# Optimization experiments

Hardware: AMD Instinct MI355X
Metric: run time of the kernel (lower is better)

Reference implementation:

```python
import jax, jax.numpy as jnp
import numpy as np

N_USER, N_FOOD, N_ING, N_CAT, N_HAB = 50000, 30000, 20000, 5000, 10000
N_NODES = N_USER + N_FOOD + N_ING + N_CAT + N_HAB  # 115000
N_REL = 8
COMMON = 128
HIDDEN = 128
N_CLASSES = 2
N_EDGES = 1500000


def setup_inputs() -> dict:
    key = jax.random.key(0)
    ks = jax.random.split(key, 24)

    def lin(k, din, dout):
        k1, k2 = jax.random.split(k)
        s = 1.0 / np.sqrt(din)
        W = jax.random.uniform(k1, (din, dout), jnp.float32, -s, s)
        b = jax.random.uniform(k2, (dout,), jnp.float32, -s, s)
        return W, b

    Wu, bu = lin(ks[0], 256, COMMON)
    Wf, bf = lin(ks[1], 512, COMMON)
    Wi, bi = lin(ks[2], 128, COMMON)
    Wc, bc = lin(ks[3], 64, COMMON)
    Wh, bh = lin(ks[4], 64, COMMON)

    s1 = 1.0 / np.sqrt(COMMON)
    W1 = jax.random.uniform(ks[5], (N_REL, COMMON, HIDDEN), jnp.float32, -s1, s1)
    root1 = jax.random.uniform(ks[6], (COMMON, HIDDEN), jnp.float32, -s1, s1)
    b1 = jnp.zeros((HIDDEN,), jnp.float32)

    s2 = 1.0 / np.sqrt(HIDDEN)
    W2 = jax.random.uniform(ks[7], (N_REL, HIDDEN, N_CLASSES), jnp.float32, -s2, s2)
    root2 = jax.random.uniform(ks[8], (HIDDEN, N_CLASSES), jnp.float32, -s2, s2)
    b2 = jnp.zeros((N_CLASSES,), jnp.float32)

    return {
        "x_user": jax.random.normal(ks[9], (N_USER, 256), jnp.float32),
        "x_food": jax.random.normal(ks[10], (N_FOOD, 512), jnp.float32),
        "x_ingredient": jax.random.normal(ks[11], (N_ING, 128), jnp.float32),
        "x_category": jax.random.normal(ks[12], (N_CAT, 64), jnp.float32),
        "x_habit": jax.random.normal(ks[13], (N_HAB, 64), jnp.float32),
        "Wu": Wu, "bu": bu, "Wf": Wf, "bf": bf, "Wi": Wi, "bi": bi,
        "Wc": Wc, "bc": bc, "Wh": Wh, "bh": bh,
        "W1": W1, "root1": root1, "b1": b1,
        "W2": W2, "root2": root2, "b2": b2,
        "edge_index": jax.random.randint(ks[14], (2, N_EDGES), 0, N_NODES, jnp.int64),
        "edge_type": jax.random.randint(ks[15], (N_EDGES,), 0, N_REL, jnp.int64),
    }


def rgcn_conv(x, src, dst, etype, W, root, bias):
    # x: [N, Din]; W: [R, Din, Dout]. Per-relation node transform, then
    # per-edge gather + per-(dst, relation) mean aggregation (PyG RGCNConv, aggr='mean').
    N = x.shape[0]
    R = W.shape[0]
    h = jnp.einsum('nd,rdf->nrf', x, W)            # [N, R, Dout]
    msgs = h[src, etype]                           # [E, Dout]
    seg = dst * R + etype                          # combined (dst, relation) segment id
    sums = jax.ops.segment_sum(msgs, seg, num_segments=N * R)
    cnt = jax.ops.segment_sum(jnp.ones((src.shape[0],), x.dtype), seg, num_segments=N * R)
    mean = sums / jnp.maximum(cnt, 1.0)[:, None]   # [N*R, Dout]
    agg = mean.reshape(N, R, -1).sum(axis=1)       # sum over relations
    return agg + x @ root + bias


def reference(x_user, x_food, x_ingredient, x_category, x_habit,
              Wu, bu, Wf, bf, Wi, bi, Wc, bc, Wh, bh,
              W1, root1, b1, W2, root2, b2,
              edge_index, edge_type):
    x_all = jnp.concatenate([
        x_user @ Wu + bu,
        x_food @ Wf + bf,
        x_ingredient @ Wi + bi,
        x_category @ Wc + bc,
        x_habit @ Wh + bh,
    ], axis=0)                                     # [N, COMMON]
    src, dst = edge_index[0], edge_index[1]
    x = rgcn_conv(x_all, src, dst, edge_type, W1, root1, b1)
    x = jax.nn.relu(x)                             # dropout is identity in eval mode
    x = rgcn_conv(x, src, dst, edge_type, W2, root2, b2)
    return jax.nn.log_softmax(x, axis=1)
```

## Files before the change

### kernel.cpp

```cpp
#include <hip/hip_runtime.h>
#include <hip/hip_bf16.h>
#include <math.h>

#define NU 50000
#define NFOOD 30000
#define NING 20000
#define NCAT 5000
#define NHAB 10000
#define NNODES 115000
#define NCHUNK 14375
#define NREL 8
#define NSEG (NNODES * NREL)
#define NEDGE 1500000
#define SCAN_B 256

typedef __attribute__((ext_vector_type(8))) short short8;
typedef __attribute__((ext_vector_type(4))) float f32x4;

static inline size_t alignup(size_t x) { return (x + 255) & ~(size_t)255; }

__device__ inline float bf16_bits_to_f32(unsigned short u) {
  return __uint_as_float(((unsigned)u) << 16);
}
__device__ inline unsigned short f32_to_bf16_bits(float f) {
  unsigned u = __float_as_uint(f);
  unsigned r = u + 0x7fffu + ((u >> 16) & 1u);
  return (unsigned short)(r >> 16);
}
__device__ inline unsigned pack_bf16x2(float lo, float hi) {
  return (unsigned)f32_to_bf16_bits(lo) | ((unsigned)f32_to_bf16_bits(hi) << 16);
}

template <bool A_F32, bool OUT_BF16, bool RELU_OUT>
__global__ __launch_bounds__(256) void mfma_gemm(
    const void* __restrict__ Ain, const unsigned short* __restrict__ Bt, int ldB,
    const float* __restrict__ bias, void* __restrict__ Cv, int ldC, int Nstore,
    int M, int N, int K) {
  __shared__ char As[128 * 128];
  __shared__ char Bs[128 * 128];
  const int tid = threadIdx.x;
  const int lane = tid & 63;
  const int wv = tid >> 6;
  const int bm = blockIdx.y * 128;
  const int bn = blockIdx.x * 128;
  f32x4 acc[2][8] = {};

  for (int k0 = 0; k0 < K; k0 += 64) {
    if (A_F32) {
      const float* A = (const float*)Ain;
#pragma unroll
      for (int it = 0; it < 4; ++it) {
        int u = it * 256 + tid;
        int m = u >> 3, c = u & 7;
        int mg = bm + m; if (mg >= M) mg = M - 1;
        const float4* src = (const float4*)(A + (size_t)mg * K + k0 + c * 8);
        float4 lo4 = src[0], hi4 = src[1];
        unsigned q0 = pack_bf16x2(lo4.x, lo4.y);
        unsigned q1 = pack_bf16x2(lo4.z, lo4.w);
        unsigned q2 = pack_bf16x2(hi4.x, hi4.y);
        unsigned q3 = pack_bf16x2(hi4.z, hi4.w);
        int off = m * 128 + ((c * 16) ^ ((m & 7) << 4));
        *(int4*)(As + off) = make_int4(q0, q1, q2, q3);
      }
    } else {
      const unsigned short* A = (const unsigned short*)Ain;
#pragma unroll
      for (int it = 0; it < 4; ++it) {
        int u = it * 256 + tid;
        int m = u >> 3, c = u & 7;
        int mg = bm + m; if (mg >= M) mg = M - 1;
        int4 v = *(const int4*)((const char*)(A + (size_t)mg * K + k0) + c * 16);
        int off = m * 128 + ((c * 16) ^ ((m & 7) << 4));
        *(int4*)(As + off) = v;
      }
    }
#pragma unroll
    for (int it = 0; it < 4; ++it) {
      int u = it * 256 + tid;
      int n = u >> 3, c = u & 7;
      int4 v = *(const int4*)((const char*)(Bt + (size_t)(bn + n) * ldB + k0) + c * 16);
      int off = n * 128 + ((c * 16) ^ ((n & 7) << 4));
      *(int4*)(Bs + off) = v;
    }
    __syncthreads();
#pragma unroll
    for (int kk = 0; kk < 2; ++kk) {
      int kbyte = kk * 64 + ((lane >> 4) << 4);
      short8 af[2];
#pragma unroll
      for (int mi = 0; mi < 2; ++mi) {
        int m = wv * 32 + mi * 16 + (lane & 15);
        af[mi] = *(const short8*)(As + m * 128 + (kbyte ^ ((m & 7) << 4)));
      }
#pragma unroll
      for (int ni = 0; ni < 8; ++ni) {
        int n = ni * 16 + (lane & 15);
        short8 bf = *(const short8*)(Bs + n * 128 + (kbyte ^ ((n & 7) << 4)));
#pragma unroll
        for (int mi = 0; mi < 2; ++mi)
          acc[mi][ni] = __builtin_amdgcn_mfma_f32_16x16x32_bf16(af[mi], bf, acc[mi][ni], 0, 0, 0);
      }
    }
    __syncthreads();
  }
#pragma unroll
  for (int mi = 0; mi < 2; ++mi) {
#pragma unroll
    for (int r = 0; r < 4; ++r) {
      int row = bm + wv * 32 + mi * 16 + ((lane >> 4) << 2) + r;
      if (row < M) {
#pragma unroll
        for (int ni = 0; ni < 8; ++ni) {
          int col = bn + ni * 16 + (lane & 15);
          if (col < Nstore) {
            float v = acc[mi][ni][r] + (bias ? bias[col] : 0.f);
            if (RELU_OUT) v = fmaxf(v, 0.f);
            if (OUT_BF16)
              ((unsigned short*)Cv)[(size_t)row * ldC + col] = f32_to_bf16_bits(v);
            else
              ((float*)Cv)[(size_t)row * ldC + col] = v;
          }
        }
      }
    }
  }
}

struct ProjP {
  const float *A0, *A1, *A2, *A3, *A4;
  const float *b0, *b1, *b2, *b3, *b4;
  int t1, t2, t3, t4;
};

__global__ __launch_bounds__(256) void proj_all(ProjP P, const unsigned short* __restrict__ Wp,
                                                unsigned short* __restrict__ x_all) {
  __shared__ char As[128 * 128];
  __shared__ char Bs[128 * 128];
  const int by = blockIdx.y;
  const int tid = threadIdx.x;
  const int lane = tid & 63;
  const int wv = tid >> 6;
  const float* A; const float* bias;
  int M, K, Woff, tile0; long Coff;
  if (by < P.t1)      { A = P.A0; bias = P.b0; M = NU;    K = 256; Woff = 0;      Coff = 0;                 tile0 = 0; }
  else if (by < P.t2) { A = P.A1; bias = P.b1; M = NFOOD; K = 512; Woff = 32768;  Coff = (long)NU * 128;    tile0 = P.t1; }
  else if (by < P.t3) { A = P.A2; bias = P.b2; M = NING;  K = 128; Woff = 98304;  Coff = (long)(NU+NFOOD)*128; tile0 = P.t2; }
  else if (by < P.t4) { A = P.A3; bias = P.b3; M = NCAT;  K = 64;  Woff = 114688; Coff = (long)(NU+NFOOD+NING)*128; tile0 = P.t3; }
  else                { A = P.A4; bias = P.b4; M = NHAB;  K = 64;  Woff = 122880; Coff = (long)(NU+NFOOD+NING+NCAT)*128; tile0 = P.t4; }
  const unsigned short* Bt = Wp + Woff;
  const int bm = (by - tile0) * 128;
  f32x4 acc[2][8] = {};

  for (int k0 = 0; k0 < K; k0 += 64) {
#pragma unroll
    for (int it = 0; it < 4; ++it) {
      int u = it * 256 + tid;
      int m = u >> 3, c = u & 7;
      int mg = bm + m; if (mg >= M) mg = M - 1;
      const float4* src = (const float4*)(A + (size_t)mg * K + k0 + c * 8);
      float4 lo4 = src[0], hi4 = src[1];
      unsigned q0 = pack_bf16x2(lo4.x, lo4.y);
      unsigned q1 = pack_bf16x2(lo4.z, lo4.w);
      unsigned q2 = pack_bf16x2(hi4.x, hi4.y);
      unsigned q3 = pack_bf16x2(hi4.z, hi4.w);
      int off = m * 128 + ((c * 16) ^ ((m & 7) << 4));
      *(int4*)(As + off) = make_int4(q0, q1, q2, q3);
    }
#pragma unroll
    for (int it = 0; it < 4; ++it) {
      int u = it * 256 + tid;
      int n = u >> 3, c = u & 7;
      int4 v = *(const int4*)((const char*)(Bt + (size_t)n * K + k0) + c * 16);
      int off = n * 128 + ((c * 16) ^ ((n & 7) << 4));
      *(int4*)(Bs + off) = v;
    }
    __syncthreads();
#pragma unroll
    for (int kk = 0; kk < 2; ++kk) {
      int kbyte = kk * 64 + ((lane >> 4) << 4);
      short8 af[2];
#pragma unroll
      for (int mi = 0; mi < 2; ++mi) {
        int m = wv * 32 + mi * 16 + (lane & 15);
        af[mi] = *(const short8*)(As + m * 128 + (kbyte ^ ((m & 7) << 4)));
      }
#pragma unroll
      for (int ni = 0; ni < 8; ++ni) {
        int n = ni * 16 + (lane & 15);
        short8 bf = *(const short8*)(Bs + n * 128 + (kbyte ^ ((n & 7) << 4)));
#pragma unroll
        for (int mi = 0; mi < 2; ++mi)
          acc[mi][ni] = __builtin_amdgcn_mfma_f32_16x16x32_bf16(af[mi], bf, acc[mi][ni], 0, 0, 0);
      }
    }
    __syncthreads();
  }
#pragma unroll
  for (int mi = 0; mi < 2; ++mi) {
#pragma unroll
    for (int r = 0; r < 4; ++r) {
      int row = bm + wv * 32 + mi * 16 + ((lane >> 4) << 2) + r;
      if (row < M) {
#pragma unroll
        for (int ni = 0; ni < 8; ++ni) {
          int col = ni * 16 + (lane & 15);
          float v = acc[mi][ni][r] + bias[col];
          x_all[Coff + (size_t)row * 128 + col] = f32_to_bf16_bits(v);
        }
      }
    }
  }
}

__global__ __launch_bounds__(256) void l1_gemm(
    const unsigned short* __restrict__ M9, const unsigned short* __restrict__ xall,
    const unsigned short* __restrict__ W1rT, const float* __restrict__ b1,
    unsigned short* __restrict__ x1, int d0, int Mc) {
  __shared__ char As[128 * 128];
  __shared__ char Bs[128 * 128];
  const int tid = threadIdx.x;
  const int lane = tid & 63;
  const int wv = tid >> 6;
  const int bm = blockIdx.y * 128;
  f32x4 acc[2][8] = {};

  for (int k0 = 0; k0 < 1152; k0 += 64) {
#pragma unroll
    for (int it = 0; it < 4; ++it) {
      int u = it * 256 + tid;
      int m = u >> 3, c = u & 7;
      int mg = bm + m; if (mg >= Mc) mg = Mc - 1;
      const char* src;
      if (k0 < 1024) src = (const char*)(M9 + (size_t)mg * 1024 + k0) + c * 16;
      else src = (const char*)(xall + (size_t)(d0 + mg) * 128 + (k0 - 1024)) + c * 16;
      int4 v = *(const int4*)src;
      int off = m * 128 + ((c * 16) ^ ((m & 7) << 4));
      *(int4*)(As + off) = v;
    }
#pragma unroll
    for (int it = 0; it < 4; ++it) {
      int u = it * 256 + tid;
      int n = u >> 3, c = u & 7;
      int4 v = *(const int4*)((const char*)(W1rT + (size_t)n * 1152 + k0) + c * 16);
      int off = n * 128 + ((c * 16) ^ ((n & 7) << 4));
      *(int4*)(Bs + off) = v;
    }
    __syncthreads();
#pragma unroll
    for (int kk = 0; kk < 2; ++kk) {
      int kbyte = kk * 64 + ((lane >> 4) << 4);
      short8 af[2];
#pragma unroll
      for (int mi = 0; mi < 2; ++mi) {
        int m = wv * 32 + mi * 16 + (lane & 15);
        af[mi] = *(const short8*)(As + m * 128 + (kbyte ^ ((m & 7) << 4)));
      }
#pragma unroll
      for (int ni = 0; ni < 8; ++ni) {
        int n = ni * 16 + (lane & 15);
        short8 bf = *(const short8*)(Bs + n * 128 + (kbyte ^ ((n & 7) << 4)));
#pragma unroll
        for (int mi = 0; mi < 2; ++mi)
          acc[mi][ni] = __builtin_amdgcn_mfma_f32_16x16x32_bf16(af[mi], bf, acc[mi][ni], 0, 0, 0);
      }
    }
    __syncthreads();
  }
#pragma unroll
  for (int mi = 0; mi < 2; ++mi) {
#pragma unroll
    for (int r = 0; r < 4; ++r) {
      int row = bm + wv * 32 + mi * 16 + ((lane >> 4) << 2) + r;
      if (row < Mc) {
#pragma unroll
        for (int ni = 0; ni < 8; ++ni) {
          int col = ni * 16 + (lane & 15);
          float v = fmaxf(acc[mi][ni][r] + b1[col], 0.f);
          x1[(size_t)(d0 + row) * 128 + col] = f32_to_bf16_bits(v);
        }
      }
    }
  }
}

__global__ void build_all(const float* __restrict__ Wu, const float* __restrict__ Wf,
                          const float* __restrict__ Wi, const float* __restrict__ Wc,
                          const float* __restrict__ Wh, const float* __restrict__ W1,
                          const float* __restrict__ root1, const float* __restrict__ W2,
                          const float* __restrict__ root2,
                          unsigned short* __restrict__ Wp,
                          unsigned short* __restrict__ W1rT,
                          unsigned short* __restrict__ B2pad,
                          int* __restrict__ cnt_dt) {
  const int T0 = 32768, T1 = T0 + 65536, T2 = T1 + 16384, T3 = T2 + 8192, T4 = T3 + 8192,
            T5 = T4 + 147456, T6 = T5 + 16384, T7 = T6 + NSEG;
  int i = blockIdx.x * blockDim.x + threadIdx.x;
  int stride = gridDim.x * blockDim.x;
  for (; i < T7; i += stride) {
    if (i < T0) {
      int n = i / 256, k = i - n * 256;
      Wp[i] = f32_to_bf16_bits(Wu[(size_t)k * 128 + n]);
    } else if (i < T1) {
      int j = i - T0; int n = j / 512, k = j - n * 512;
      Wp[i] = f32_to_bf16_bits(Wf[(size_t)k * 128 + n]);
    } else if (i < T2) {
      int j = i - T1; int n = j >> 7, k = j & 127;
      Wp[i] = f32_to_bf16_bits(Wi[(size_t)k * 128 + n]);
    } else if (i < T3) {
      int j = i - T2; int n = j >> 6, k = j & 63;
      Wp[i] = f32_to_bf16_bits(Wc[(size_t)k * 128 + n]);
    } else if (i < T4) {
      int j = i - T3; int n = j >> 6, k = j & 63;
      Wp[i] = f32_to_bf16_bits(Wh[(size_t)k * 128 + n]);
    } else if (i < T5) {
      int j = i - T4; int f = j / 1152, c = j - f * 1152;
      float v;
      if (c < 1024) { int t = c >> 7, k = c & 127; v = W1[((size_t)t * 128 + k) * 128 + f]; }
      else { int k = c - 1024; v = root1[(size_t)k * 128 + f]; }
      W1rT[j] = f32_to_bf16_bits(v);
    } else if (i < T6) {
      int j = i - T5; int n = j >> 7, k = j & 127;
      float v = 0.f;
      if (n < 16) v = W2[((size_t)(n >> 1) * 128 + k) * 2 + (n & 1)];
      else if (n < 18) v = root2[(size_t)k * 2 + (n - 16)];
      B2pad[j] = f32_to_bf16_bits(v);
    } else {
      cnt_dt[i - T6] = 0;
    }
  }
}

__global__ void count_dt_xcd(const int* __restrict__ ei, const int* __restrict__ et,
                             int* __restrict__ cnt_dt) {
  int cls = blockIdx.x & 7;
  unsigned lo = cls * NCHUNK, hi = lo + NCHUNK;
  int e = (blockIdx.x >> 3) * blockDim.x + threadIdx.x;
  int stride = (gridDim.x >> 3) * blockDim.x;
  for (; e < NEDGE; e += stride) {
    unsigned d = (unsigned)ei[NEDGE + e]; if (d >= NNODES) d = 0;
    if (d < lo || d >= hi) continue;
    unsigned t = (unsigned)et[e]; if (t >= NREL) t = 0;
    atomicAdd(cnt_dt + d * NREL + t, 1);
  }
}

__global__ void scan_block(const int* __restrict__ in, int* __restrict__ out,
                           int* __restrict__ bsum, int n) {
  __shared__ int s[SCAN_B];
  int i = blockIdx.x * SCAN_B + threadIdx.x;
  int x = (i < n) ? in[i] : 0;
  s[threadIdx.x] = x;
  __syncthreads();
  for (int d = 1; d < SCAN_B; d <<= 1) {
    int v = (threadIdx.x >= d) ? s[threadIdx.x - d] : 0;
    __syncthreads();
    s[threadIdx.x] += v;
    __syncthreads();
  }
  if (i < n) out[i] = s[threadIdx.x] - x;
  if (threadIdx.x == SCAN_B - 1) bsum[blockIdx.x] = s[threadIdx.x];
}

__global__ void scan_mid(const int* __restrict__ bsumA, int* __restrict__ bsumAs, int nb) {
  __shared__ int s[256];
  __shared__ int carry;
  if (threadIdx.x == 0) carry = 0;
  __syncthreads();
  for (int c0 = 0; c0 < nb; c0 += 256) {
    int i = c0 + threadIdx.x;
    int x = (i < nb) ? bsumA[i] : 0;
    s[threadIdx.x] = x;
    __syncthreads();
    for (int d = 1; d < 256; d <<= 1) {
      int v = (threadIdx.x >= d) ? s[threadIdx.x - d] : 0;
      __syncthreads();
      s[threadIdx.x] += v;
      __syncthreads();
    }
    if (i < nb) bsumAs[i] = carry + s[threadIdx.x] - x;
    __syncthreads();
    if (threadIdx.x == 255) carry += s[255];
    __syncthreads();
  }
}

__global__ void scan_apply2(int* __restrict__ rp2, const int* __restrict__ lvl1,
                            int* __restrict__ slot, int n) {
  int i = blockIdx.x * blockDim.x + threadIdx.x;
  if (i >= n) return;
  int v = rp2[i] + lvl1[i >> 8];
  rp2[i] = v;
  slot[i] = v;
}

__global__ void scatter_edges_xcd(const int* __restrict__ ei, const int* __restrict__ et,
                                  int* __restrict__ slot, unsigned* __restrict__ packed) {
  int cls = blockIdx.x & 7;
  unsigned lo = cls * NCHUNK, hi = lo + NCHUNK;
  int e = (blockIdx.x >> 3) * blockDim.x + threadIdx.x;
  int stride = (gridDim.x >> 3) * blockDim.x;
  for (; e < NEDGE; e += stride) {
    unsigned d = (unsigned)ei[NEDGE + e]; if (d >= NNODES) d = 0;
    if (d < lo || d >= hi) continue;
    unsigned s = (unsigned)ei[e];  if (s >= NNODES) s = 0;
    unsigned t = (unsigned)et[e];  if (t >= NREL)  t = 0;
    int pos = atomicAdd(slot + d * NREL + t, 1);
    packed[pos] = s;
  }
}

__global__ __launch_bounds__(256) void gather_rounds(
    const int* __restrict__ rp2, const unsigned* __restrict__ packed,
    const int4* __restrict__ xu, unsigned* __restrict__ M9, int d0, int d1) {
  const int lane = threadIdx.x & 63;
  const int qtr = lane >> 4;
  const int sub = lane & 15;
  int wid = (blockIdx.x * blockDim.x + threadIdx.x) >> 6;
  int nw = (gridDim.x * blockDim.x) >> 6;
  for (int p0 = d0 + wid * 4; p0 < d1; p0 += nw * 4) {
    int d = p0 + qtr;
    bool valid = (d < d1);
    int bi = (valid ? d : d0) * NREL;
    int b[9];
#pragma unroll
    for (int q = 0; q < 9; ++q)
      b[q] = (bi + q == NSEG) ? NEDGE : rp2[bi + q];
    int len[8];
    int mx = 0;
#pragma unroll
    for (int q = 0; q < 8; ++q) {
      len[q] = valid ? (b[q + 1] - b[q]) : 0;
      mx = len[q] > mx ? len[q] : mx;
    }
    float a[8][8];
#pragma unroll
    for (int q = 0; q < 8; ++q)
#pragma unroll
      for (int j = 0; j < 8; ++j) a[q][j] = 0.f;
    for (int r = 0; r < mx; ++r) {
#pragma unroll
      for (int q = 0; q < 8; ++q) {
        if (r < len[q]) {
          int4 v = xu[(size_t)packed[b[q] + r] * 16 + sub];
          unsigned u0 = (unsigned)v.x, u1 = (unsigned)v.y;
          unsigned u2 = (unsigned)v.z, u3 = (unsigned)v.w;
          a[q][0] += bf16_bits_to_f32((unsigned short)(u0 & 0xffffu));
          a[q][1] += bf16_bits_to_f32((unsigned short)(u0 >> 16));
          a[q][2] += bf16_bits_to_f32((unsigned short)(u1 & 0xffffu));
          a[q][3] += bf16_bits_to_f32((unsigned short)(u1 >> 16));
          a[q][4] += bf16_bits_to_f32((unsigned short)(u2 & 0xffffu));
          a[q][5] += bf16_bits_to_f32((unsigned short)(u2 >> 16));
          a[q][6] += bf16_bits_to_f32((unsigned short)(u3 & 0xffffu));
          a[q][7] += bf16_bits_to_f32((unsigned short)(u3 >> 16));
        }
      }
    }
    if (valid) {
      unsigned* rowp = M9 + (size_t)(d - d0) * 512;
#pragma unroll
      for (int q = 0; q < 8; ++q) {
        float w = 1.0f / (float)(len[q] > 0 ? len[q] : 1);
        uint4 o;
        o.x = pack_bf16x2(a[q][0] * w, a[q][1] * w);
        o.y = pack_bf16x2(a[q][2] * w, a[q][3] * w);
        o.z = pack_bf16x2(a[q][4] * w, a[q][5] * w);
        o.w = pack_bf16x2(a[q][6] * w, a[q][7] * w);
        *(uint4*)(rowp + q * 64 + sub * 4) = o;
      }
    }
  }
}

__global__ void fused_out(const int* __restrict__ rp2, const unsigned* __restrict__ packed,
                          const float* __restrict__ h2, const float* __restrict__ b2,
                          float* __restrict__ out) {
  int gt = blockIdx.x * blockDim.x + threadIdx.x;
  int d = gt >> 2;
  int l4 = gt & 3;
  if (d >= NNODES) return;
  float z0 = 0.f, z1 = 0.f;
#pragma unroll
  for (int k = 0; k < 2; ++k) {
    int t = l4 * 2 + k;
    int i = d * NREL + t;
    int beg = rp2[i];
    int end = (i == NSEG - 1) ? NEDGE : rp2[i + 1];
    float s0 = 0.f, s1 = 0.f;
    for (int e = beg; e < end; ++e) {
      unsigned s = packed[e];
      s0 += h2[(size_t)s * 18 + t * 2];
      s1 += h2[(size_t)s * 18 + t * 2 + 1];
    }
    int c = end - beg;
    float w = 1.0f / (float)(c > 0 ? c : 1);
    z0 += s0 * w;
    z1 += s1 * w;
  }
  z0 += __shfl_xor(z0, 1, 4); z0 += __shfl_xor(z0, 2, 4);
  z1 += __shfl_xor(z1, 1, 4); z1 += __shfl_xor(z1, 2, 4);
  if (l4 == 0) {
    z0 += h2[(size_t)d * 18 + 16] + b2[0];
    z1 += h2[(size_t)d * 18 + 17] + b2[1];
    float m = fmaxf(z0, z1);
    float l = m + logf(expf(z0 - m) + expf(z1 - m));
    out[(size_t)d * 2 + 0] = z0 - l;
    out[(size_t)d * 2 + 1] = z1 - l;
  }
}

__global__ void fill_sentinel(float* __restrict__ out, int n, float v) {
  int i = blockIdx.x * blockDim.x + threadIdx.x;
  if (i < n) out[i] = v;
}

extern "C" void kernel_launch(void* const* d_in, const int* in_sizes, int n_in,
                              void* d_out, int out_size, void* d_ws, size_t ws_size,
                              hipStream_t stream) {
  const float* x_user = (const float*)d_in[0];
  const float* x_food = (const float*)d_in[1];
  const float* x_ing  = (const float*)d_in[2];
  const float* x_cat  = (const float*)d_in[3];
  const float* x_hab  = (const float*)d_in[4];
  const float* Wu = (const float*)d_in[5];  const float* bu  = (const float*)d_in[6];
  const float* Wf = (const float*)d_in[7];  const float* bfo = (const float*)d_in[8];
  const float* Wi = (const float*)d_in[9];  const float* bi  = (const float*)d_in[10];
  const float* Wc = (const float*)d_in[11]; const float* bc  = (const float*)d_in[12];
  const float* Wh = (const float*)d_in[13]; const float* bh  = (const float*)d_in[14];
  const float* W1 = (const float*)d_in[15]; const float* root1 = (const float*)d_in[16];
  const float* b1 = (const float*)d_in[17];
  const float* W2 = (const float*)d_in[18]; const float* root2 = (const float*)d_in[19];
  const float* b2 = (const float*)d_in[20];
  const int* ei = (const int*)d_in[21];
  const int* et = (const int*)d_in[22];
  (void)in_sizes; (void)n_in;

  dim3 blk(256);
  const int NB_A = (NSEG + SCAN_B - 1) / SCAN_B;

  char* ws = (char*)d_ws;
  size_t off = 0;
  unsigned short* x_all = (unsigned short*)(ws + off); off += alignup((size_t)NNODES * 128 * 2);
  unsigned short* x1    = (unsigned short*)(ws + off); off += alignup((size_t)NNODES * 128 * 2);
  int* cnt_dt = (int*)(ws + off);        off += alignup((size_t)NSEG * 4);
  int* rp2 = (int*)(ws + off);           off += alignup((size_t)NSEG * 4);
  int* slot = (int*)(ws + off);          off += alignup((size_t)NSEG * 4);
  unsigned* packed = (unsigned*)(ws + off); off += alignup((size_t)NEDGE * 4);
  int* bsumA = (int*)(ws + off);         off += alignup((size_t)4096 * 4);
  int* bsumAs = (int*)(ws + off);        off += alignup((size_t)4096 * 4);
  unsigned short* Wp = (unsigned short*)(ws + off);   off += alignup((size_t)131072 * 2);
  unsigned short* W1rT = (unsigned short*)(ws + off); off += alignup((size_t)128 * 1152 * 2);
  unsigned short* B2pad = (unsigned short*)(ws + off); off += alignup((size_t)128 * 128 * 2);
  float* h2 = (float*)(ws + off);        off += alignup((size_t)NNODES * 18 * 4);
  size_t base = off;

  int NCH = 0;
  for (int cand = 1; cand <= 16; cand <<= 1) {
    size_t ch = ((size_t)NNODES + cand - 1) / cand;
    if (base + alignup(ch * 1024 * 2) <= ws_size) { NCH = cand; break; }
  }
  if (NCH == 0) {
    fill_sentinel<<<(out_size + 255) / 256, blk, 0, stream>>>((float*)d_out, out_size, -777.0f);
    return;
  }
  unsigned short* M9 = (unsigned short*)(ws + base);
  const int CH = (NNODES + NCH - 1) / NCH;

  build_all<<<2048, blk, 0, stream>>>(Wu, Wf, Wi, Wc, Wh, W1, root1, W2, root2,
                                      Wp, W1rT, B2pad, cnt_dt);

  {
    ProjP P;
    P.A0 = x_user; P.A1 = x_food; P.A2 = x_ing; P.A3 = x_cat; P.A4 = x_hab;
    P.b0 = bu; P.b1 = bfo; P.b2 = bi; P.b3 = bc; P.b4 = bh;
    P.t1 = 391; P.t2 = 391 + 235; P.t3 = 391 + 235 + 157; P.t4 = 391 + 235 + 157 + 40;
    int ntiles = P.t4 + 79;
    proj_all<<<dim3(1, ntiles), blk, 0, stream>>>(P, Wp, x_all);
  }

  count_dt_xcd<<<2048, blk, 0, stream>>>(ei, et, cnt_dt);
  scan_block<<<NB_A, SCAN_B, 0, stream>>>(cnt_dt, rp2, bsumA, NSEG);
  scan_mid<<<1, 256, 0, stream>>>(bsumA, bsumAs, NB_A);
  scan_apply2<<<NB_A, SCAN_B, 0, stream>>>(rp2, bsumAs, slot, NSEG);
  scatter_edges_xcd<<<2048, blk, 0, stream>>>(ei, et, slot, packed);

  for (int c = 0; c < NCH; ++c) {
    int d0 = c * CH;
    int d1 = (d0 + CH < NNODES) ? d0 + CH : NNODES;
    int Mc = d1 - d0;
    int groups = (Mc + 3) / 4;
    int gblocks = (groups + 3) / 4;
    gather_rounds<<<gblocks, blk, 0, stream>>>(rp2, packed, (const int4*)x_all,
                                               (unsigned*)M9, d0, d1);
    dim3 g(1, (Mc + 127) / 128);
    l1_gemm<<<g, blk, 0, stream>>>(M9, x_all, W1rT, b1, x1, d0, Mc);
  }

  { dim3 g(1, (NNODES + 127) / 128);
    mfma_gemm<false, false, false><<<g, blk, 0, stream>>>(x1, B2pad, 128, nullptr, (void*)h2, 18, 18, NNODES, 128, 128); }

  fused_out<<<(NNODES * 4 + 255) / 256, blk, 0, stream>>>(rp2, packed, h2, b2, (float*)d_out);
}
```

Before: 479.4 us.

## Fuse layer-2 projection GEMM into layer-1 GEMM epilogue via shared memory

The layer-1 GEMM now keeps its ReLU'd bf16 output tile in shared memory, reusing the A/B staging buffers. It multiplies that tile by the padded layer-2 weights loaded into LDS and writes h2 directly. This removes the x1 intermediate (write plus reread of about 29 MB) and one kernel launch. In exchange it adds LDS usage and extra per-block work after the main loop, which may reduce occupancy.

```diff
diff --git a/kernel.cpp b/kernel.cpp
--- a/kernel.cpp
+++ b/kernel.cpp
@@ -29,101 +29,6 @@
 }
 __device__ inline unsigned pack_bf16x2(float lo, float hi) {
   return (unsigned)f32_to_bf16_bits(lo) | ((unsigned)f32_to_bf16_bits(hi) << 16);
-}
-
-template <bool A_F32, bool OUT_BF16, bool RELU_OUT>
-__global__ __launch_bounds__(256) void mfma_gemm(
-    const void* __restrict__ Ain, const unsigned short* __restrict__ Bt, int ldB,
-    const float* __restrict__ bias, void* __restrict__ Cv, int ldC, int Nstore,
-    int M, int N, int K) {
-  __shared__ char As[128 * 128];
-  __shared__ char Bs[128 * 128];
-  const int tid = threadIdx.x;
-  const int lane = tid & 63;
-  const int wv = tid >> 6;
-  const int bm = blockIdx.y * 128;
-  const int bn = blockIdx.x * 128;
-  f32x4 acc[2][8] = {};
-
-  for (int k0 = 0; k0 < K; k0 += 64) {
-    if (A_F32) {
-      const float* A = (const float*)Ain;
-#pragma unroll
-      for (int it = 0; it < 4; ++it) {
-        int u = it * 256 + tid;
-        int m = u >> 3, c = u & 7;
-        int mg = bm + m; if (mg >= M) mg = M - 1;
-        const float4* src = (const float4*)(A + (size_t)mg * K + k0 + c * 8);
-        float4 lo4 = src[0], hi4 = src[1];
-        unsigned q0 = pack_bf16x2(lo4.x, lo4.y);
-        unsigned q1 = pack_bf16x2(lo4.z, lo4.w);
-        unsigned q2 = pack_bf16x2(hi4.x, hi4.y);
-        unsigned q3 = pack_bf16x2(hi4.z, hi4.w);
-        int off = m * 128 + ((c * 16) ^ ((m & 7) << 4));
-        *(int4*)(As + off) = make_int4(q0, q1, q2, q3);
-      }
-    } else {
-      const unsigned short* A = (const unsigned short*)Ain;
-#pragma unroll
-      for (int it = 0; it < 4; ++it) {
-        int u = it * 256 + tid;
-        int m = u >> 3, c = u & 7;
-        int mg = bm + m; if (mg >= M) mg = M - 1;
-        int4 v = *(const int4*)((const char*)(A + (size_t)mg * K + k0) + c * 16);
-        int off = m * 128 + ((c * 16) ^ ((m & 7) << 4));
-        *(int4*)(As + off) = v;
-      }
-    }
-#pragma unroll
-    for (int it = 0; it < 4; ++it) {
-      int u = it * 256 + tid;
-      int n = u >> 3, c = u & 7;
-      int4 v = *(const int4*)((const char*)(Bt + (size_t)(bn + n) * ldB + k0) + c * 16);
-      int off = n * 128 + ((c * 16) ^ ((n & 7) << 4));
-      *(int4*)(Bs + off) = v;
-    }
-    __syncthreads();
-#pragma unroll
-    for (int kk = 0; kk < 2; ++kk) {
-      int kbyte = kk * 64 + ((lane >> 4) << 4);
-      short8 af[2];
-#pragma unroll
-      for (int mi = 0; mi < 2; ++mi) {
-        int m = wv * 32 + mi * 16 + (lane & 15);
-        af[mi] = *(const short8*)(As + m * 128 + (kbyte ^ ((m & 7) << 4)));
-      }
-#pragma unroll
-      for (int ni = 0; ni < 8; ++ni) {
-        int n = ni * 16 + (lane & 15);
-        short8 bf = *(const short8*)(Bs + n * 128 + (kbyte ^ ((n & 7) << 4)));
-#pragma unroll
-        for (int mi = 0; mi < 2; ++mi)
-          acc[mi][ni] = __builtin_amdgcn_mfma_f32_16x16x32_bf16(af[mi], bf, acc[mi][ni], 0, 0, 0);
-      }
-    }
-    __syncthreads();
-  }
-#pragma unroll
-  for (int mi = 0; mi < 2; ++mi) {
-#pragma unroll
-    for (int r = 0; r < 4; ++r) {
-      int row = bm + wv * 32 + mi * 16 + ((lane >> 4) << 2) + r;
-      if (row < M) {
-#pragma unroll
-        for (int ni = 0; ni < 8; ++ni) {
-          int col = bn + ni * 16 + (lane & 15);
-          if (col < Nstore) {
-            float v = acc[mi][ni][r] + (bias ? bias[col] : 0.f);
-            if (RELU_OUT) v = fmaxf(v, 0.f);
-            if (OUT_BF16)
-              ((unsigned short*)Cv)[(size_t)row * ldC + col] = f32_to_bf16_bits(v);
-            else
-              ((float*)Cv)[(size_t)row * ldC + col] = v;
-          }
-        }
-      }
-    }
-  }
 }
 
 struct ProjP {
@@ -215,14 +120,24 @@
 __global__ __launch_bounds__(256) void l1_gemm(
     const unsigned short* __restrict__ M9, const unsigned short* __restrict__ xall,
     const unsigned short* __restrict__ W1rT, const float* __restrict__ b1,
-    unsigned short* __restrict__ x1, int d0, int Mc) {
+    const unsigned short* __restrict__ B2pad, float* __restrict__ h2,
+    int d0, int Mc) {
   __shared__ char As[128 * 128];
   __shared__ char Bs[128 * 128];
+  __shared__ char B2s[32 * 256];
   const int tid = threadIdx.x;
   const int lane = tid & 63;
   const int wv = tid >> 6;
+  const int r16 = lane & 15;
+  const int q0 = lane >> 4;
   const int bm = blockIdx.y * 128;
   f32x4 acc[2][8] = {};
+
+  for (int i = tid; i < 512; i += 256) {
+    int n = i >> 4, g = i & 15;
+    int4 v = *(const int4*)((const char*)(B2pad + (size_t)n * 128) + g * 16);
+    *(int4*)(B2s + n * 256 + ((g * 16) ^ ((n & 7) << 4))) = v;
+  }
 
   for (int k0 = 0; k0 < 1152; k0 += 64) {
 #pragma unroll
@@ -248,16 +163,16 @@
     __syncthreads();
 #pragma unroll
     for (int kk = 0; kk < 2; ++kk) {
-      int kbyte = kk * 64 + ((lane >> 4) << 4);
+      int kbyte = kk * 64 + (q0 << 4);
       short8 af[2];
 #pragma unroll
       for (int mi = 0; mi < 2; ++mi) {
-        int m = wv * 32 + mi * 16 + (lane & 15);
+        int m = wv * 32 + mi * 16 + r16;
         af[mi] = *(const short8*)(As + m * 128 + (kbyte ^ ((m & 7) << 4)));
       }
 #pragma unroll
       for (int ni = 0; ni < 8; ++ni) {
-        int n = ni * 16 + (lane & 15);
+        int n = ni * 16 + r16;
         short8 bf = *(const short8*)(Bs + n * 128 + (kbyte ^ ((n & 7) << 4)));
 #pragma unroll
         for (int mi = 0; mi < 2; ++mi)
@@ -266,18 +181,55 @@
     }
     __syncthreads();
   }
+
 #pragma unroll
   for (int mi = 0; mi < 2; ++mi) {
 #pragma unroll
     for (int r = 0; r < 4; ++r) {
-      int row = bm + wv * 32 + mi * 16 + ((lane >> 4) << 2) + r;
-      if (row < Mc) {
-#pragma unroll
-        for (int ni = 0; ni < 8; ++ni) {
-          int col = ni * 16 + (lane & 15);
-          float v = fmaxf(acc[mi][ni][r] + b1[col], 0.f);
-          x1[(size_t)(d0 + row) * 128 + col] = f32_to_bf16_bits(v);
-        }
+      int row = wv * 32 + mi * 16 + q0 * 4 + r;
+      char* base = (row < 64) ? As : Bs;
+      int rb = (row & 63) * 256;
+#pragma unroll
+      for (int ni = 0; ni < 8; ++ni) {
+        int col = ni * 16 + r16;
+        float v = fmaxf(acc[mi][ni][r] + b1[col], 0.f);
+        int byte = rb + ((((col >> 3) << 4) ^ ((row & 7) << 4)) | ((col & 7) << 1));
+        *(unsigned short*)(base + byte) = f32_to_bf16_bits(v);
+      }
+    }
+  }
+  __syncthreads();
+
+  f32x4 acc2[2][2] = {};
+#pragma unroll
+  for (int kk = 0; kk < 4; ++kk) {
+    int kbyte = kk * 64 + (q0 << 4);
+    short8 af[2];
+#pragma unroll
+    for (int mi = 0; mi < 2; ++mi) {
+      int m = wv * 32 + mi * 16 + r16;
+      const char* base = (m < 64) ? As : Bs;
+      af[mi] = *(const short8*)(base + (m & 63) * 256 + (kbyte ^ ((m & 7) << 4)));
+    }
+#pragma unroll
+    for (int ni = 0; ni < 2; ++ni) {
+      int n = ni * 16 + r16;
+      short8 bf = *(const short8*)(B2s + n * 256 + (kbyte ^ ((n & 7) << 4)));
+#pragma unroll
+      for (int mi = 0; mi < 2; ++mi)
+        acc2[mi][ni] = __builtin_amdgcn_mfma_f32_16x16x32_bf16(af[mi], bf, acc2[mi][ni], 0, 0, 0);
+    }
+  }
+#pragma unroll
+  for (int mi = 0; mi < 2; ++mi) {
+#pragma unroll
+    for (int ni = 0; ni < 2; ++ni) {
+#pragma unroll
+      for (int r = 0; r < 4; ++r) {
+        int row = bm + wv * 32 + mi * 16 + q0 * 4 + r;
+        int col = ni * 16 + r16;
+        if (row < Mc && col < 18)
+          h2[(size_t)(d0 + row) * 18 + col] = acc2[mi][ni][r];
       }
     }
   }
@@ -540,7 +492,6 @@
   char* ws = (char*)d_ws;
   size_t off = 0;
   unsigned short* x_all = (unsigned short*)(ws + off); off += alignup((size_t)NNODES * 128 * 2);
-  unsigned short* x1    = (unsigned short*)(ws + off); off += alignup((size_t)NNODES * 128 * 2);
   int* cnt_dt = (int*)(ws + off);        off += alignup((size_t)NSEG * 4);
   int* rp2 = (int*)(ws + off);           off += alignup((size_t)NSEG * 4);
   int* slot = (int*)(ws + off);          off += alignup((size_t)NSEG * 4);
@@ -592,11 +543,8 @@
     gather_rounds<<<gblocks, blk, 0, stream>>>(rp2, packed, (const int4*)x_all,
                                                (unsigned*)M9, d0, d1);
     dim3 g(1, (Mc + 127) / 128);
-    l1_gemm<<<g, blk, 0, stream>>>(M9, x_all, W1rT, b1, x1, d0, Mc);
-  }
-
-  { dim3 g(1, (NNODES + 127) / 128);
-    mfma_gemm<false, false, false><<<g, blk, 0, stream>>>(x1, B2pad, 128, nullptr, (void*)h2, 18, 18, NNODES, 128, 128); }
+    l1_gemm<<<g, blk, 0, stream>>>(M9, x_all, W1rT, b1, B2pad, h2, d0, Mc);
+  }
 
   fused_out<<<(NNODES * 4 + 255) / 256, blk, 0, stream>>>(rp2, packed, h2, b2, (float*)d_out);
 }
```

New measurement: 457.2 us, median of 2. 4.6% less time.
